# Performance work log

Measured on AMD Instinct MI355X. Metric: run time of the kernel, lower is better.

## Reference

```python
import jax, jax.numpy as jnp
import numpy as np

N_NODES = 100000
N_FEAT = 512
HIDDEN = 16
N_CLASSES = 7
N_EDGES = 3200000


def gcn_conv(x, W, b, src, dst, num_nodes):
    """GCNConv: add self-loops, symmetric deg^-1/2 normalization, linear, aggregate."""
    loop = jnp.arange(num_nodes, dtype=src.dtype)
    src2 = jnp.concatenate([src, loop])  # [E+N]
    dst2 = jnp.concatenate([dst, loop])
    ones = jnp.ones(src2.shape[0], dtype=x.dtype)
    deg = jax.ops.segment_sum(ones, dst2, num_segments=num_nodes)  # in-degree incl. self-loop
    dinv = jnp.where(deg > 0, jax.lax.rsqrt(deg), 0.0)
    norm = dinv[src2] * dinv[dst2]  # [E+N]
    h = x @ W  # [N, out] -- transform before gather (small out dim)
    msg = h[src2] * norm[:, None]  # gather + scale
    out = jax.ops.segment_sum(msg, dst2, num_segments=num_nodes)  # scatter-add
    return out + b


def setup_inputs() -> dict:
    key = jax.random.key(0)
    k1, k2, k3, k4, k5 = jax.random.split(key, 5)
    x = jax.random.normal(k1, (N_NODES, N_FEAT), dtype=jnp.float32)
    edge_index = jax.random.randint(k2, (2, N_EDGES), 0, N_NODES, dtype=jnp.int64)
    # Glorot init like PyG GCNConv
    W1 = jax.random.normal(k3, (N_FEAT, HIDDEN), dtype=jnp.float32) * np.sqrt(2.0 / (N_FEAT + HIDDEN))
    b1 = jnp.zeros((HIDDEN,), dtype=jnp.float32)
    W2 = jax.random.normal(k4, (HIDDEN, N_CLASSES), dtype=jnp.float32) * np.sqrt(2.0 / (HIDDEN + N_CLASSES))
    b2 = jnp.zeros((N_CLASSES,), dtype=jnp.float32)
    return {"x": x, "edge_index": edge_index, "W1": W1, "b1": b1, "W2": W2, "b2": b2}


def reference(x, edge_index, W1, b1, W2, b2):
    src, dst = edge_index[0], edge_index[1]
    h = gcn_conv(x, W1, b1, src, dst, N_NODES)
    h = jax.nn.relu(h)
    # F.dropout(training=self.training): identity in eval mode (deterministic reference)
    h = gcn_conv(h, W2, b2, src, dst, N_NODES)
    return jax.nn.log_softmax(h, axis=1)
```

## Files before the change

kernel.cpp:

```cpp
#include <hip/hip_runtime.h>
#include <math.h>

#define N_NODES   100000
#define N_FEAT    512
#define HIDDEN    16
#define N_CLASSES 7
#define N_EDGES   3200000

#define BSHIFT 7
#define BNODES 128
#define BMASK  127
#define NBUK   782
#define CHUNK  16384
#define NCHUNK 196
#define CAP    6144

__device__ __forceinline__ float bf_lo(unsigned int p) { return __uint_as_float(p << 16); }
__device__ __forceinline__ float bf_hi(unsigned int p) { return __uint_as_float(p & 0xffff0000u); }
__device__ __forceinline__ unsigned int pack_bf2(float a, float b) {
    unsigned int ua = __float_as_uint(a); ua += 0x7fffu + ((ua >> 16) & 1u);
    unsigned int ub = __float_as_uint(b); ub += 0x7fffu + ((ub >> 16) & 1u);
    return (ua >> 16) | (ub & 0xffff0000u);
}


__global__ void k_zero_b(int* __restrict__ btot) {
    int i = threadIdx.x;
    if (i < NBUK) btot[i] = 0;
}

__global__ __launch_bounds__(256) void k_bhist(const int* __restrict__ dst,
                                               int* __restrict__ btot) {
    __shared__ int h[NBUK];
    int tid = threadIdx.x;
    for (int i = tid; i < NBUK; i += 256) h[i] = 0;
    __syncthreads();
    int base = blockIdx.x * CHUNK;
    for (int i = tid; i < CHUNK; i += 256) {
        int e = base + i;
        if (e < N_EDGES) atomicAdd(&h[dst[e] >> BSHIFT], 1);
    }
    __syncthreads();
    for (int i = tid; i < NBUK; i += 256)
        if (h[i]) atomicAdd(&btot[i], h[i]);
}

__global__ void k_bscan(const int* __restrict__ btot, int* __restrict__ gbase,
                        int* __restrict__ gcur) {
    __shared__ int sd[1024];
    int t = threadIdx.x;
    int v = (t < NBUK) ? btot[t] : 0;
    sd[t] = v;
    __syncthreads();
    for (int off = 1; off < 1024; off <<= 1) {
        int a = (t >= off) ? sd[t - off] : 0;
        __syncthreads();
        sd[t] += a;
        __syncthreads();
    }
    if (t < NBUK) {
        int ex = sd[t] - v;
        gbase[t] = ex;
        gcur[t]  = ex;
    }
}

__global__ __launch_bounds__(256) void k_bscatter(const int* __restrict__ src,
                                                  const int* __restrict__ dst,
                                                  int* __restrict__ gcur,
                                                  int* __restrict__ entries) {
    __shared__ int h[NBUK];
    __shared__ int lb[NBUK];
    int tid = threadIdx.x;
    for (int i = tid; i < NBUK; i += 256) h[i] = 0;
    __syncthreads();
    int base = blockIdx.x * CHUNK;
    for (int i = tid; i < CHUNK; i += 256) {
        int e = base + i;
        if (e < N_EDGES) atomicAdd(&h[dst[e] >> BSHIFT], 1);
    }
    __syncthreads();
    for (int i = tid; i < NBUK; i += 256) {
        int c = h[i];
        lb[i] = c ? atomicAdd(&gcur[i], c) : 0;
        h[i] = 0;
    }
    __syncthreads();
    for (int i = tid; i < CHUNK; i += 256) {
        int e = base + i;
        if (e < N_EDGES) {
            int d = dst[e];
            int b = d >> BSHIFT;
            int pos = lb[b] + atomicAdd(&h[b], 1);
            entries[pos] = src[e] | ((d & BMASK) << 17);
        }
    }
}


__global__ __launch_bounds__(512) void k_nodesort(int* __restrict__ entries,
                                                  const int* __restrict__ btot,
                                                  const int* __restrict__ gbase,
                                                  float* __restrict__ dinv,
                                                  int* __restrict__ nodeptr) {
    __shared__ int ebuf[CAP];
    __shared__ int hcnt[BNODES];
    __shared__ int hincl[BNODES];
    __shared__ int hcur[BNODES];
    int tid = threadIdx.x;
    int bk = blockIdx.x;
    int cnt = btot[bk], base = gbase[bk];
    if (cnt > CAP) cnt = CAP;
    if (tid < BNODES) hcnt[tid] = 0;
    __syncthreads();
    for (int i = tid; i < cnt; i += 512) {
        int en = entries[base + i];
        ebuf[i] = en;
        atomicAdd(&hcnt[en >> 17], 1);
    }
    __syncthreads();
    if (tid < BNODES) hincl[tid] = hcnt[tid];
    __syncthreads();
    for (int off = 1; off < BNODES; off <<= 1) {
        int v = 0;
        if (tid < BNODES && tid >= off) v = hincl[tid - off];
        __syncthreads();
        if (tid < BNODES) hincl[tid] += v;
        __syncthreads();
    }
    if (tid < BNODES) {
        int excl = hincl[tid] - hcnt[tid];
        hcur[tid] = excl;
        int n = bk * BNODES + tid;
        if (n < N_NODES) {
            nodeptr[n] = base + excl;
            dinv[n]    = rsqrtf((float)(hcnt[tid] + 1));
        } else if (n == N_NODES) {
            nodeptr[n] = base + excl;
        }
    }
    __syncthreads();
    for (int i = tid; i < cnt; i += 512) {
        int en = ebuf[i];
        int pos = atomicAdd(&hcur[en >> 17], 1);
        entries[base + pos] = en & 0x1FFFF;
    }
}


__global__ __launch_bounds__(256) void k_gemm1(const float* __restrict__ x,
                                               const float* __restrict__ W1,
                                               const float* __restrict__ dinv,
                                               unsigned int* __restrict__ hs1b) {
    __shared__ float wl[512 * 17];
    int tid = threadIdx.x;
    for (int idx = tid; idx < N_FEAT * HIDDEN; idx += 256) {
        int col = idx >> 4, o = idx & 15;
        wl[col * 17 + o] = W1[idx];
    }
    __syncthreads();

    int lane = tid & 15;
    int row  = blockIdx.x * 16 + (tid >> 4);
    const float4* xr = (const float4*)(x + (size_t)row * N_FEAT);

    float acc[16];
#pragma unroll
    for (int o = 0; o < 16; o++) acc[o] = 0.f;

#pragma unroll
    for (int i = 0; i < 8; i++) {
        int col = i * 64 + lane * 4;
        float4 xv = xr[col >> 2];
#pragma unroll
        for (int j = 0; j < 4; j++) {
            float xj = (&xv.x)[j];
            const float* wr = &wl[(col + j) * 17];
#pragma unroll
            for (int o = 0; o < 16; o++) acc[o] += xj * wr[o];
        }
    }

#pragma unroll
    for (int m = 1; m < 16; m <<= 1) {
#pragma unroll
        for (int o = 0; o < 16; o++) acc[o] += __shfl_xor(acc[o], m, 64);
    }

    if (lane == 0) {
        float dn = dinv[row];
        uint4* outp = (uint4*)(hs1b + (size_t)row * 8);
        outp[0] = make_uint4(pack_bf2(acc[0] * dn,  acc[1] * dn),
                             pack_bf2(acc[2] * dn,  acc[3] * dn),
                             pack_bf2(acc[4] * dn,  acc[5] * dn),
                             pack_bf2(acc[6] * dn,  acc[7] * dn));
        outp[1] = make_uint4(pack_bf2(acc[8] * dn,  acc[9] * dn),
                             pack_bf2(acc[10] * dn, acc[11] * dn),
                             pack_bf2(acc[12] * dn, acc[13] * dn),
                             pack_bf2(acc[14] * dn, acc[15] * dn));
    }
}


__global__ __launch_bounds__(512) void k_agg1(const unsigned int* __restrict__ hs1b,
                                              const int* __restrict__ srt,
                                              const int* __restrict__ nodeptr,
                                              const float* __restrict__ dinv,
                                              const float* __restrict__ b1,
                                              const float* __restrict__ W2,
                                              unsigned int* __restrict__ hs2b) {
    __shared__ float w2l[HIDDEN * N_CLASSES];
    __shared__ float b1l[HIDDEN];
    int tid = threadIdx.x;
    if (tid < HIDDEN * N_CLASSES) w2l[tid] = W2[tid];
    if (tid < HIDDEN) b1l[tid] = b1[tid];
    __syncthreads();

    int bk = blockIdx.x;
    int g = tid >> 3, j = tid & 7;

#pragma unroll
    for (int rep = 0; rep < 2; rep++) {
        int l = g + rep * 64;
        int n = bk * BNODES + l;
        float t[7] = {0.f, 0.f, 0.f, 0.f, 0.f, 0.f, 0.f};
        float dn = 0.f;
        if (n < N_NODES) {
            int p0 = nodeptr[n], p1 = nodeptr[n + 1];
            float aL0 = 0, aH0 = 0, aL1 = 0, aH1 = 0;
            float aL2 = 0, aH2 = 0, aL3 = 0, aH3 = 0;
            int e = p0;
            for (; e + 4 <= p1; e += 4) {
                int s0 = srt[e], s1 = srt[e + 1], s2 = srt[e + 2], s3 = srt[e + 3];
                unsigned int v0 = hs1b[(size_t)s0 * 8 + j];
                unsigned int v1 = hs1b[(size_t)s1 * 8 + j];
                unsigned int v2 = hs1b[(size_t)s2 * 8 + j];
                unsigned int v3 = hs1b[(size_t)s3 * 8 + j];
                aL0 += bf_lo(v0); aH0 += bf_hi(v0);
                aL1 += bf_lo(v1); aH1 += bf_hi(v1);
                aL2 += bf_lo(v2); aH2 += bf_hi(v2);
                aL3 += bf_lo(v3); aH3 += bf_hi(v3);
            }
            for (; e < p1; e++) {
                unsigned int v = hs1b[(size_t)srt[e] * 8 + j];
                aL0 += bf_lo(v); aH0 += bf_hi(v);
            }
            unsigned int sv = hs1b[(size_t)n * 8 + j];
            float accL = aL0 + aL1 + aL2 + aL3 + bf_lo(sv);
            float accH = aH0 + aH1 + aH2 + aH3 + bf_hi(sv);
            dn = dinv[n];
            float z0 = fmaxf(dn * accL + b1l[2 * j],     0.f);
            float z1 = fmaxf(dn * accH + b1l[2 * j + 1], 0.f);
            const float* wr0 = &w2l[(2 * j) * 7];
            const float* wr1 = &w2l[(2 * j + 1) * 7];
#pragma unroll
            for (int q = 0; q < 7; q++) t[q] = z0 * wr0[q] + z1 * wr1[q];
        }
#pragma unroll
        for (int m = 1; m < 8; m <<= 1) {
#pragma unroll
            for (int q = 0; q < 7; q++) t[q] += __shfl_xor(t[q], m, 64);
        }
        if (j == 0 && n < N_NODES) {
            uint4* o = (uint4*)(hs2b + (size_t)n * 4);
            o[0] = make_uint4(pack_bf2(dn * t[0], dn * t[1]),
                              pack_bf2(dn * t[2], dn * t[3]),
                              pack_bf2(dn * t[4], dn * t[5]),
                              pack_bf2(dn * t[6], 0.f));
        }
    }
}


__global__ __launch_bounds__(512) void k_agg2(const unsigned int* __restrict__ hs2b,
                                              const int* __restrict__ srt,
                                              const int* __restrict__ nodeptr,
                                              const float* __restrict__ dinv,
                                              const float* __restrict__ b2,
                                              float* __restrict__ out) {
    int tid = threadIdx.x;
    int g = tid >> 2, j = tid & 3;
    int bk = blockIdx.x;
    int n = bk * BNODES + g;
    bool valid = (n < N_NODES);
    float lL = -3.4e38f, lH = -3.4e38f;
    if (valid) {
        int p0 = nodeptr[n], p1 = nodeptr[n + 1];
        float aL0 = 0, aH0 = 0, aL1 = 0, aH1 = 0;
        float aL2 = 0, aH2 = 0, aL3 = 0, aH3 = 0;
        int e = p0;
        for (; e + 4 <= p1; e += 4) {
            int s0 = srt[e], s1 = srt[e + 1], s2 = srt[e + 2], s3 = srt[e + 3];
            unsigned int v0 = hs2b[(size_t)s0 * 4 + j];
            unsigned int v1 = hs2b[(size_t)s1 * 4 + j];
            unsigned int v2 = hs2b[(size_t)s2 * 4 + j];
            unsigned int v3 = hs2b[(size_t)s3 * 4 + j];
            aL0 += bf_lo(v0); aH0 += bf_hi(v0);
            aL1 += bf_lo(v1); aH1 += bf_hi(v1);
            aL2 += bf_lo(v2); aH2 += bf_hi(v2);
            aL3 += bf_lo(v3); aH3 += bf_hi(v3);
        }
        for (; e < p1; e++) {
            unsigned int v = hs2b[(size_t)srt[e] * 4 + j];
            aL0 += bf_lo(v); aH0 += bf_hi(v);
        }
        unsigned int sv = hs2b[(size_t)n * 4 + j];
        float accL = aL0 + aL1 + aL2 + aL3 + bf_lo(sv);
        float accH = aH0 + aH1 + aH2 + aH3 + bf_hi(sv);
        float dn = dinv[n];
        lL = dn * accL + b2[2 * j];
        int c = 2 * j + 1;
        lH = (c < 7) ? (dn * accH + b2[c]) : -3.4e38f;
    }
    float m = fmaxf(lL, lH);
    m = fmaxf(m, __shfl_xor(m, 1, 64));
    m = fmaxf(m, __shfl_xor(m, 2, 64));
    float s = 0.f;
    if (valid) {
        s = expf(lL - m);
        if (2 * j + 1 < 7) s += expf(lH - m);
    }
    s += __shfl_xor(s, 1, 64);
    s += __shfl_xor(s, 2, 64);
    if (valid) {
        float ls = m + logf(s);
        out[(size_t)n * 7 + 2 * j] = lL - ls;
        if (2 * j + 1 < 7) out[(size_t)n * 7 + 2 * j + 1] = lH - ls;
    }
}


extern "C" void kernel_launch(void* const* d_in, const int* in_sizes, int n_in,
                              void* d_out, int out_size, void* d_ws, size_t ws_size,
                              hipStream_t stream) {
    const float* x  = (const float*)d_in[0];
    const int*   ei = (const int*)d_in[1];
    const float* W1 = (const float*)d_in[2];
    const float* b1 = (const float*)d_in[3];
    const float* W2 = (const float*)d_in[4];
    const float* b2 = (const float*)d_in[5];
    float* out = (float*)d_out;

    const int* src = ei;
    const int* dst = ei + N_EDGES;

    char* w = (char*)d_ws;
    int*          btot    = (int*)(w + 0);
    int*          gbase   = (int*)(w + 4096);
    int*          gcur    = (int*)(w + 8192);
    float*        dinv    = (float*)(w + 12288);
    int*          nodeptr = (int*)(w + 412672);
    unsigned int* hs1b    = (unsigned int*)(w + 815104);
    unsigned int* hs2b    = (unsigned int*)(w + 4016128);
    int*          entries = (int*)(w + 5617664);

    k_zero_b  <<<1, 1024, 0, stream>>>(btot);
    k_bhist   <<<NCHUNK, 256, 0, stream>>>(dst, btot);
    k_bscan   <<<1, 1024, 0, stream>>>(btot, gbase, gcur);
    k_bscatter<<<NCHUNK, 256, 0, stream>>>(src, dst, gcur, entries);
    k_nodesort<<<NBUK, 512, 0, stream>>>(entries, btot, gbase, dinv, nodeptr);
    k_gemm1   <<<N_NODES / 16, 256, 0, stream>>>(x, W1, dinv, hs1b);
    k_agg1    <<<NBUK, 512, 0, stream>>>(hs1b, entries, nodeptr, dinv, b1, W2, hs2b);
    k_agg2    <<<NBUK, 512, 0, stream>>>(hs2b, entries, nodeptr, dinv, b2, out);
}
```

Measured before the change: 520.5 us.

## Use bf16 MFMA for first GEMM and per-chunk histograms for bucket sort

```diff
diff --git a/kernel.cpp b/kernel.cpp
--- a/kernel.cpp
+++ b/kernel.cpp
@@ -15,6 +15,9 @@
 #define NCHUNK 196
 #define CAP    6144
 
+typedef short v8s __attribute__((ext_vector_type(8)));
+typedef float v4f __attribute__((ext_vector_type(4)));
+
 __device__ __forceinline__ float bf_lo(unsigned int p) { return __uint_as_float(p << 16); }
 __device__ __forceinline__ float bf_hi(unsigned int p) { return __uint_as_float(p & 0xffff0000u); }
 __device__ __forceinline__ unsigned int pack_bf2(float a, float b) {
@@ -24,13 +27,8 @@
 }
 
 
-__global__ void k_zero_b(int* __restrict__ btot) {
-    int i = threadIdx.x;
-    if (i < NBUK) btot[i] = 0;
-}
-
-__global__ __launch_bounds__(256) void k_bhist(const int* __restrict__ dst,
-                                               int* __restrict__ btot) {
+__global__ __launch_bounds__(256) void k_hist(const int* __restrict__ dst,
+                                              int* __restrict__ hglob) {
     __shared__ int h[NBUK];
     int tid = threadIdx.x;
     for (int i = tid; i < NBUK; i += 256) h[i] = 0;
@@ -42,15 +40,20 @@
     }
     __syncthreads();
     for (int i = tid; i < NBUK; i += 256)
-        if (h[i]) atomicAdd(&btot[i], h[i]);
-}
-
-__global__ void k_bscan(const int* __restrict__ btot, int* __restrict__ gbase,
-                        int* __restrict__ gcur) {
+        hglob[blockIdx.x * NBUK + i] = h[i];
+}
+
+
+__global__ __launch_bounds__(1024) void k_scan(const int* __restrict__ hglob,
+                                               int* __restrict__ btot,
+                                               int* __restrict__ gbase,
+                                               int* __restrict__ hpre) {
     __shared__ int sd[1024];
     int t = threadIdx.x;
-    int v = (t < NBUK) ? btot[t] : 0;
-    sd[t] = v;
+    int tot = 0;
+    if (t < NBUK)
+        for (int c = 0; c < NCHUNK; c++) tot += hglob[c * NBUK + t];
+    sd[t] = (t < NBUK) ? tot : 0;
     __syncthreads();
     for (int off = 1; off < 1024; off <<= 1) {
         int a = (t >= off) ? sd[t - off] : 0;
@@ -59,39 +62,37 @@
         __syncthreads();
     }
     if (t < NBUK) {
-        int ex = sd[t] - v;
+        int ex = sd[t] - tot;
+        btot[t] = tot;
         gbase[t] = ex;
-        gcur[t]  = ex;
-    }
-}
-
-__global__ __launch_bounds__(256) void k_bscatter(const int* __restrict__ src,
-                                                  const int* __restrict__ dst,
-                                                  int* __restrict__ gcur,
-                                                  int* __restrict__ entries) {
-    __shared__ int h[NBUK];
+        int run = ex;
+        for (int c = 0; c < NCHUNK; c++) {
+            hpre[c * NBUK + t] = run;
+            run += hglob[c * NBUK + t];
+        }
+    }
+}
+
+
+__global__ __launch_bounds__(256) void k_scatter(const int* __restrict__ src,
+                                                 const int* __restrict__ dst,
+                                                 const int* __restrict__ hpre,
+                                                 int* __restrict__ entries) {
     __shared__ int lb[NBUK];
-    int tid = threadIdx.x;
-    for (int i = tid; i < NBUK; i += 256) h[i] = 0;
+    __shared__ int cur[NBUK];
+    int tid = threadIdx.x;
+    for (int i = tid; i < NBUK; i += 256) {
+        lb[i] = hpre[blockIdx.x * NBUK + i];
+        cur[i] = 0;
+    }
     __syncthreads();
     int base = blockIdx.x * CHUNK;
-    for (int i = tid; i < CHUNK; i += 256) {
-        int e = base + i;
-        if (e < N_EDGES) atomicAdd(&h[dst[e] >> BSHIFT], 1);
-    }
-    __syncthreads();
-    for (int i = tid; i < NBUK; i += 256) {
-        int c = h[i];
-        lb[i] = c ? atomicAdd(&gcur[i], c) : 0;
-        h[i] = 0;
-    }
-    __syncthreads();
     for (int i = tid; i < CHUNK; i += 256) {
         int e = base + i;
         if (e < N_EDGES) {
             int d = dst[e];
             int b = d >> BSHIFT;
-            int pos = lb[b] + atomicAdd(&h[b], 1);
+            int pos = lb[b] + atomicAdd(&cur[b], 1);
             entries[pos] = src[e] | ((d & BMASK) << 17);
         }
     }
@@ -152,52 +153,74 @@
                                                const float* __restrict__ W1,
                                                const float* __restrict__ dinv,
                                                unsigned int* __restrict__ hs1b) {
-    __shared__ float wl[512 * 17];
-    int tid = threadIdx.x;
-    for (int idx = tid; idx < N_FEAT * HIDDEN; idx += 256) {
-        int col = idx >> 4, o = idx & 15;
-        wl[col * 17 + o] = W1[idx];
-    }
-    __syncthreads();
-
-    int lane = tid & 15;
-    int row  = blockIdx.x * 16 + (tid >> 4);
-    const float4* xr = (const float4*)(x + (size_t)row * N_FEAT);
-
-    float acc[16];
-#pragma unroll
-    for (int o = 0; o < 16; o++) acc[o] = 0.f;
-
-#pragma unroll
-    for (int i = 0; i < 8; i++) {
-        int col = i * 64 + lane * 4;
-        float4 xv = xr[col >> 2];
-#pragma unroll
-        for (int j = 0; j < 4; j++) {
-            float xj = (&xv.x)[j];
-            const float* wr = &wl[(col + j) * 17];
-#pragma unroll
-            for (int o = 0; o < 16; o++) acc[o] += xj * wr[o];
-        }
-    }
-
-#pragma unroll
-    for (int m = 1; m < 16; m <<= 1) {
-#pragma unroll
-        for (int o = 0; o < 16; o++) acc[o] += __shfl_xor(acc[o], m, 64);
-    }
-
-    if (lane == 0) {
-        float dn = dinv[row];
-        uint4* outp = (uint4*)(hs1b + (size_t)row * 8);
-        outp[0] = make_uint4(pack_bf2(acc[0] * dn,  acc[1] * dn),
-                             pack_bf2(acc[2] * dn,  acc[3] * dn),
-                             pack_bf2(acc[4] * dn,  acc[5] * dn),
-                             pack_bf2(acc[6] * dn,  acc[7] * dn));
-        outp[1] = make_uint4(pack_bf2(acc[8] * dn,  acc[9] * dn),
-                             pack_bf2(acc[10] * dn, acc[11] * dn),
-                             pack_bf2(acc[12] * dn, acc[13] * dn),
-                             pack_bf2(acc[14] * dn, acc[15] * dn));
+    __shared__ unsigned int wfrag[16 * 64 * 4];
+    __shared__ unsigned int atile[64 * 68];
+
+    int tid = threadIdx.x;
+    int wave = tid >> 6, lane = tid & 63;
+    int row0 = blockIdx.x * 64;
+    int m = lane & 15, quad = lane >> 4;
+
+    {
+        int q0 = tid * 4;
+#pragma unroll
+        for (int qq = 0; qq < 4; qq++) {
+            int q = q0 + qq;
+            int s = q >> 6, l = q & 63;
+            int n = l & 15, kb = s * 32 + (l >> 4) * 8;
+            unsigned int* wp = &wfrag[q * 4];
+#pragma unroll
+            for (int h = 0; h < 4; h++)
+                wp[h] = pack_bf2(W1[(kb + 2 * h) * 16 + n],
+                                 W1[(kb + 2 * h + 1) * 16 + n]);
+        }
+    }
+
+    v4f acc = {0.f, 0.f, 0.f, 0.f};
+
+    for (int c = 0; c < 4; c++) {
+        __syncthreads();
+#pragma unroll
+        for (int i = 0; i < 8; i++) {
+            int f = i * 256 + tid;
+            int r = f >> 5, c4 = f & 31;
+            int grow = row0 + r;
+            float4 xv = make_float4(0.f, 0.f, 0.f, 0.f);
+            if (grow < N_NODES)
+                xv = *(const float4*)(x + (size_t)grow * N_FEAT + c * 128 + c4 * 4);
+            unsigned int* ap = &atile[r * 68 + c4 * 2];
+            ap[0] = pack_bf2(xv.x, xv.y);
+            ap[1] = pack_bf2(xv.z, xv.w);
+        }
+        __syncthreads();
+#pragma unroll
+        for (int s = 0; s < 4; s++) {
+            v8s af = *(const v8s*)&atile[(wave * 16 + m) * 68 + s * 16 + quad * 4];
+            v8s bf = *(const v8s*)&wfrag[((c * 4 + s) * 64 + lane) * 4];
+            acc = __builtin_amdgcn_mfma_f32_16x16x32_bf16(af, bf, acc, 0, 0, 0);
+        }
+    }
+
+    __syncthreads();
+    float* dt = (float*)atile;
+    {
+        float* wdt = dt + wave * 272;
+        int col = lane & 15;
+#pragma unroll
+        for (int r = 0; r < 4; r++)
+            wdt[(quad * 4 + r) * 17 + col] = acc[r];
+    }
+    __syncthreads();
+    {
+        int row = tid >> 2, p = tid & 3;
+        int grow = row0 + row;
+        if (grow < N_NODES) {
+            float dn = dinv[grow];
+            float* wdt = dt + (row >> 4) * 272 + (row & 15) * 17 + 4 * p;
+            unsigned int d0 = pack_bf2(dn * wdt[0], dn * wdt[1]);
+            unsigned int d1 = pack_bf2(dn * wdt[2], dn * wdt[3]);
+            *(uint2*)(hs1b + (size_t)grow * 8 + 2 * p) = make_uint2(d0, d1);
+        }
     }
 }
 
@@ -257,9 +280,9 @@
             for (int q = 0; q < 7; q++) t[q] = z0 * wr0[q] + z1 * wr1[q];
         }
 #pragma unroll
-        for (int m = 1; m < 8; m <<= 1) {
-#pragma unroll
-            for (int q = 0; q < 7; q++) t[q] += __shfl_xor(t[q], m, 64);
+        for (int mk = 1; mk < 8; mk <<= 1) {
+#pragma unroll
+            for (int q = 0; q < 7; q++) t[q] += __shfl_xor(t[q], mk, 64);
         }
         if (j == 0 && n < N_NODES) {
             uint4* o = (uint4*)(hs2b + (size_t)n * 4);
@@ -309,21 +332,21 @@
         float accH = aH0 + aH1 + aH2 + aH3 + bf_hi(sv);
         float dn = dinv[n];
         lL = dn * accL + b2[2 * j];
-        int c = 2 * j + 1;
-        lH = (c < 7) ? (dn * accH + b2[c]) : -3.4e38f;
-    }
-    float m = fmaxf(lL, lH);
-    m = fmaxf(m, __shfl_xor(m, 1, 64));
-    m = fmaxf(m, __shfl_xor(m, 2, 64));
+        int cch = 2 * j + 1;
+        lH = (cch < 7) ? (dn * accH + b2[cch]) : -3.4e38f;
+    }
+    float mm = fmaxf(lL, lH);
+    mm = fmaxf(mm, __shfl_xor(mm, 1, 64));
+    mm = fmaxf(mm, __shfl_xor(mm, 2, 64));
     float s = 0.f;
     if (valid) {
-        s = expf(lL - m);
-        if (2 * j + 1 < 7) s += expf(lH - m);
+        s = expf(lL - mm);
+        if (2 * j + 1 < 7) s += expf(lH - mm);
     }
     s += __shfl_xor(s, 1, 64);
     s += __shfl_xor(s, 2, 64);
     if (valid) {
-        float ls = m + logf(s);
+        float ls = mm + logf(s);
         out[(size_t)n * 7 + 2 * j] = lL - ls;
         if (2 * j + 1 < 7) out[(size_t)n * 7 + 2 * j + 1] = lH - ls;
     }
@@ -347,19 +370,19 @@
     char* w = (char*)d_ws;
     int*          btot    = (int*)(w + 0);
     int*          gbase   = (int*)(w + 4096);
-    int*          gcur    = (int*)(w + 8192);
-    float*        dinv    = (float*)(w + 12288);
-    int*          nodeptr = (int*)(w + 412672);
-    unsigned int* hs1b    = (unsigned int*)(w + 815104);
-    unsigned int* hs2b    = (unsigned int*)(w + 4016128);
-    int*          entries = (int*)(w + 5617664);
-
-    k_zero_b  <<<1, 1024, 0, stream>>>(btot);
-    k_bhist   <<<NCHUNK, 256, 0, stream>>>(dst, btot);
-    k_bscan   <<<1, 1024, 0, stream>>>(btot, gbase, gcur);
-    k_bscatter<<<NCHUNK, 256, 0, stream>>>(src, dst, gcur, entries);
+    float*        dinv    = (float*)(w + 8192);
+    int*          nodeptr = (int*)(w + 408576);
+    int*          hglob   = (int*)(w + 808960);
+    int*          hpre    = (int*)(w + 1422336);
+    unsigned int* hs1b    = (unsigned int*)(w + 2036736);
+    unsigned int* hs2b    = (unsigned int*)(w + 5236736);
+    int*          entries = (int*)(w + 6836736);
+
+    k_hist    <<<NCHUNK, 256, 0, stream>>>(dst, hglob);
+    k_scan    <<<1, 1024, 0, stream>>>(hglob, btot, gbase, hpre);
+    k_scatter <<<NCHUNK, 256, 0, stream>>>(src, dst, hpre, entries);
     k_nodesort<<<NBUK, 512, 0, stream>>>(entries, btot, gbase, dinv, nodeptr);
-    k_gemm1   <<<N_NODES / 16, 256, 0, stream>>>(x, W1, dinv, hs1b);
+    k_gemm1   <<<1563, 256, 0, stream>>>(x, W1, dinv, hs1b);
     k_agg1    <<<NBUK, 512, 0, stream>>>(hs1b, entries, nodeptr, dinv, b1, W2, hs2b);
     k_agg2    <<<NBUK, 512, 0, stream>>>(hs2b, entries, nodeptr, dinv, b2, out);
 }
```

Result: no change. 514.7 us (-1.1%).
